# Optimization experiments

Measured on AMD Instinct MI355X. Metric: run time of the kernel, lower is better.

Reference implementation:

```python
import jax, jax.numpy as jnp
import numpy as np


def setup_inputs() -> dict:
    key = jax.random.key(0)
    ks = jax.random.split(key, 8)
    B, S, D, H, E = 4, 2048, 1024, 2048, 8
    s = 0.02  # init scale
    return {
        "x": jax.random.normal(ks[0], (B, S, D), dtype=jnp.float32),
        "gate_w": jax.random.normal(ks[1], (E, D), dtype=jnp.float32) * s,
        "w1": jax.random.normal(ks[2], (E, H, D), dtype=jnp.float32) * s,
        "b1": jnp.zeros((E, H), dtype=jnp.float32),
        "w2": jax.random.normal(ks[3], (E, H, D), dtype=jnp.float32) * s,
        "b2": jnp.zeros((E, H), dtype=jnp.float32),
        "w3": jax.random.normal(ks[4], (E, D, H), dtype=jnp.float32) * s,
        "b3": jnp.zeros((E, D), dtype=jnp.float32),
        "topk": 2,
    }


def reference(x, gate_w, w1, b1, w2, b2, w3, b3, topk):
    D = x.shape[-1]
    E = gate_w.shape[0]
    xf = x.reshape(-1, D)                      # [T, D]
    T = xf.shape[0]

    logits = xf @ gate_w.T                     # [T, E]
    vals, idx = jax.lax.top_k(logits, topk)    # [T, K]
    wts = jax.nn.softmax(vals, axis=-1)        # [T, K]

    # per-token combine weight per expert (0 if expert not in top-k)
    comb = jnp.zeros((T, E), dtype=xf.dtype).at[
        jnp.arange(T)[:, None], idx
    ].add(wts)                                 # [T, E]

    out = jnp.zeros_like(xf)
    for e in range(E):  # fixed small loop over experts
        h = (xf @ w1[e].T + b1[e]) * jax.nn.silu(xf @ w2[e].T + b2[e])  # [T, H]
        y = h @ w3[e].T + b3[e]                                           # [T, D]
        out = out + comb[:, e:e + 1] * y
    return out.reshape(x.shape)
```

## Files before the change

### kernel.cpp

```cpp
#include <hip/hip_runtime.h>
#include <hip/hip_bf16.h>
#include <stdint.h>

#define T_TOK   8192
#define D_DIM   1024
#define H_DIM   2048
#define E_EXP   8
#define NP2     4096
#define BM      256
#define CAP     (2*T_TOK + E_EXP*BM)
#define MAXMB   (CAP/BM)

using f32x4 = __attribute__((ext_vector_type(4))) float;
using s16x4 = __attribute__((ext_vector_type(4))) short;
using s16x8 = __attribute__((ext_vector_type(8))) short;

__device__ __forceinline__ short bf16_of(float f) {
  union { float f; unsigned u; } v; v.f = f;
  unsigned r = v.u + 0x7FFFu + ((v.u >> 16) & 1u);
  return (short)(r >> 16);
}
__device__ __forceinline__ float f_of_bf16(short s) {
  union { unsigned u; float f; } v; v.u = ((unsigned)(unsigned short)s) << 16;
  return v.f;
}

__device__ __forceinline__ void gload16(const void* g, void* l) {
  __builtin_amdgcn_global_load_lds(
      (const __attribute__((address_space(1))) unsigned int*)g,
      (__attribute__((address_space(3))) unsigned int*)l, 16, 0, 0);
}

__global__ __launch_bounds__(256) void conv_w12(const float* __restrict__ w1,
                                                const float* __restrict__ w2,
                                                short* __restrict__ w12b) {
  int idx = blockIdx.x * 256 + threadIdx.x;
  int e = idx >> 20;
  int rem = idx & 0xFFFFF;
  int np = rem >> 8;
  int kc = rem & 255;
  int g = np >> 5, tt = np & 31, half = tt >> 4, srow = g * 16 + (tt & 15);
  const f32x4* src = (const f32x4*)(half ? w2 : w1) + ((size_t)e * H_DIM + srow) * 256 + kc;
  f32x4 v = *src;
  s16x4 o;
  o[0] = bf16_of(v[0]); o[1] = bf16_of(v[1]); o[2] = bf16_of(v[2]); o[3] = bf16_of(v[3]);
  ((s16x4*)w12b)[idx] = o;
}

__global__ __launch_bounds__(256) void conv_w3(const float* __restrict__ w3,
                                               short* __restrict__ w3b) {
  int idx = blockIdx.x * 256 + threadIdx.x;
  f32x4 v = ((const f32x4*)w3)[idx];
  s16x4 o;
  o[0] = bf16_of(v[0]); o[1] = bf16_of(v[1]); o[2] = bf16_of(v[2]); o[3] = bf16_of(v[3]);
  ((s16x4*)w3b)[idx] = o;
}

__global__ __launch_bounds__(256) void gate_kernel(const float* __restrict__ x,
                                                   const float* __restrict__ gw,
                                                   int* __restrict__ tok_e,
                                                   float* __restrict__ gatew) {
  __shared__ float g[E_EXP * D_DIM];
  int tid = threadIdx.x;
  for (int i = tid; i < E_EXP * 256; i += 256)
    ((f32x4*)g)[i] = ((const f32x4*)gw)[i];
  __syncthreads();
  int w = tid >> 6, lane = tid & 63;
  int t = blockIdx.x * 4 + w;
  float acc[E_EXP] = {};
  const f32x4* xrow = (const f32x4*)(x + (size_t)t * D_DIM);
#pragma unroll
  for (int i = 0; i < 4; ++i) {
    f32x4 xv = xrow[lane + 64 * i];
#pragma unroll
    for (int e = 0; e < E_EXP; ++e) {
      f32x4 gv = ((const f32x4*)g)[e * 256 + lane + 64 * i];
      acc[e] += xv[0] * gv[0] + xv[1] * gv[1] + xv[2] * gv[2] + xv[3] * gv[3];
    }
  }
#pragma unroll
  for (int e = 0; e < E_EXP; ++e)
#pragma unroll
    for (int off = 1; off < 64; off <<= 1)
      acc[e] += __shfl_xor(acc[e], off);
  if (lane == 0) {
    int i0 = 0; float v0 = acc[0];
    for (int e = 1; e < E_EXP; ++e) if (acc[e] > v0) { v0 = acc[e]; i0 = e; }
    int i1 = -1; float v1 = -1e30f;
    for (int e = 0; e < E_EXP; ++e) if (e != i0 && acc[e] > v1) { v1 = acc[e]; i1 = e; }
    float z = __expf(v1 - v0);
    tok_e[2 * t] = i0; tok_e[2 * t + 1] = i1;
    gatew[2 * t] = 1.f / (1.f + z); gatew[2 * t + 1] = z / (1.f + z);
  }
}

__global__ __launch_bounds__(256) void hist_kernel(const int* __restrict__ tok_e,
                                                   int* __restrict__ counts) {
  __shared__ int bc[E_EXP];
  const int tid = threadIdx.x, lane = tid & 63;
  if (tid < E_EXP) bc[tid] = 0;
  __syncthreads();
  const int4 v = ((const int4*)tok_e)[blockIdx.x * 256 + tid];
#pragma unroll
  for (int e = 0; e < E_EXP; ++e) {
    int cnt = __popcll(__ballot(v.x == e)) + __popcll(__ballot(v.y == e)) +
              __popcll(__ballot(v.z == e)) + __popcll(__ballot(v.w == e));
    if (lane == 0 && cnt) atomicAdd(&bc[e], cnt);
  }
  __syncthreads();
  if (tid < E_EXP && bc[tid]) atomicAdd(&counts[tid], bc[tid]);
}

__global__ void scan_kernel(const int* __restrict__ counts, int* __restrict__ off,
                            int* __restrict__ mb2e, int* __restrict__ mb2row) {
  if (threadIdx.x == 0 && blockIdx.x == 0) {
    int acc = 0, mb = 0;
    for (int e = 0; e < E_EXP; ++e) {
      off[e] = acc;
      int nb = (counts[e] + BM - 1) / BM;
      for (int b = 0; b < nb; ++b) { mb2e[mb] = e; mb2row[mb] = acc + b * BM; ++mb; }
      acc += nb * BM;
    }
    off[E_EXP] = acc;
    for (; mb < MAXMB; ++mb) mb2e[mb] = -1;
  }
}

__global__ __launch_bounds__(256) void assign_kernel(const int* __restrict__ tok_e,
                                                     const int* __restrict__ off,
                                                     int* __restrict__ fill,
                                                     int* __restrict__ perm,
                                                     int* __restrict__ tok_slot) {
  __shared__ int wcnt[4][E_EXP];
  __shared__ int wbase[4][E_EXP];
  const int tid = threadIdx.x, lane = tid & 63, wid = tid >> 6;
  if (tid < 32) wcnt[tid >> 3][tid & 7] = 0;
  __syncthreads();
  const int ent = blockIdx.x * 256 + tid;
  const int e = tok_e[ent];
  int myrank = 0;
#pragma unroll
  for (int e0 = 0; e0 < E_EXP; ++e0) {
    unsigned long long m = __ballot(e == e0);
    if (e == e0) {
      myrank = __popcll(m & ((1ull << lane) - 1ull));
      if (myrank == 0) wcnt[wid][e0] = __popcll(m);
    }
  }
  __syncthreads();
  if (tid < E_EXP) {
    int tot = wcnt[0][tid] + wcnt[1][tid] + wcnt[2][tid] + wcnt[3][tid];
    int base = tot ? atomicAdd(&fill[tid], tot) : 0;
#pragma unroll
    for (int w = 0; w < 4; ++w) { wbase[w][tid] = base; base += wcnt[w][tid]; }
  }
  __syncthreads();
  const int slot = off[e] + wbase[wid][e] + myrank;
  perm[slot] = ent >> 1;
  tok_slot[ent] = slot;
}

__global__ __launch_bounds__(128) void gather_kernel(const float* __restrict__ x,
                                                     const int* __restrict__ off,
                                                     const int* __restrict__ counts,
                                                     const int* __restrict__ perm,
                                                     short* __restrict__ Xp) {
  int s = blockIdx.x, tid = threadIdx.x;
  int e = -1;
#pragma unroll
  for (int i = 0; i < E_EXP; ++i)
    if (s >= off[i] && s < off[i + 1]) { e = i; break; }
  bool valid = false; int t = 0;
  if (e >= 0) { int r = s - off[e]; if (r < counts[e]) { valid = true; t = perm[s]; } }
  s16x8 o;
  if (valid) {
    const f32x4* xr = (const f32x4*)(x + (size_t)t * D_DIM);
    f32x4 a = xr[tid * 2], b = xr[tid * 2 + 1];
    o[0] = bf16_of(a[0]); o[1] = bf16_of(a[1]); o[2] = bf16_of(a[2]); o[3] = bf16_of(a[3]);
    o[4] = bf16_of(b[0]); o[5] = bf16_of(b[1]); o[6] = bf16_of(b[2]); o[7] = bf16_of(b[3]);
  } else {
#pragma unroll
    for (int j = 0; j < 8; ++j) o[j] = 0;
  }
  *(s16x8*)(Xp + (size_t)s * D_DIM + tid * 8) = o;
}

template <int K, int EPI>
__global__ __launch_bounds__(512) void gemm256(const short* __restrict__ A,
                                               const short* __restrict__ Bw,
                                               const int* __restrict__ mb2e,
                                               const int* __restrict__ mb2row,
                                               const float* __restrict__ biasA,
                                               const float* __restrict__ biasB,
                                               short* __restrict__ Out) {
  constexpr int NFULL = (EPI == 0) ? NP2 : D_DIM;
  constexpr int OUTLD = (EPI == 0) ? H_DIM : D_DIM;
  constexpr int KB = K * 2;
  constexpr int NT = K / 32;

  const int mb = blockIdx.y;
  const int e = mb2e[mb];
  if (e < 0) return;
  const int row0 = mb2row[mb];
  const int bn = blockIdx.x;

  __shared__ alignas(16) char lds[3 * 32768];

  const int tid = threadIdx.x;
  const int lane = tid & 63;
  const int wid = tid >> 6;
  const int wr = wid >> 2;
  const int wc = wid & 3;

  const char* gA = (const char*)(A + (size_t)row0 * K);
  const char* gB = (const char*)(Bw + ((size_t)e * NFULL + (size_t)bn * BM) * K);

  const int srow0 = tid >> 2, spq = tid & 3;

  f32x4 acc[8][4] = {};

  auto stage = [&](int kt, int buf, int which) {
    const char* g = which ? gB : gA;
    char* l = lds + buf * 32768 + which * 16384;
#pragma unroll
    for (int rnd = 0; rnd < 2; ++rnd) {
      const int row = rnd * 128 + srow0;
      const int lq = spq ^ ((row >> 1) & 3);
      gload16(g + (size_t)row * KB + kt * 64 + lq * 16,
              l + rnd * 8192 + tid * 16);
    }
  };

  stage(0, 0, 0); stage(0, 0, 1);
  stage(1, 1, 0); stage(1, 1, 1);
  asm volatile("s_waitcnt vmcnt(4)" ::: "memory");
  __builtin_amdgcn_s_barrier();
  __builtin_amdgcn_sched_barrier(0);

  const int qsw = (((lane >> 4) ^ ((lane >> 1) & 3)) << 4);
  const int arow = wr * 128 + (lane & 15);
  const int brow = wc * 64 + (lane & 15);

  int bc = 0;
  int b2 = 2;
  for (int t = 0; t < NT; ++t) {
    const char* bufb = lds + bc * 32768;
    const char* pa = bufb + arow * 64 + qsw;
    const char* pb = bufb + 16384 + brow * 64 + qsw;
    s16x8 av[4], bv[4];
#pragma unroll
    for (int f = 0; f < 4; ++f) bv[f] = *(const s16x8*)(pb + f * 1024);
#pragma unroll
    for (int f = 0; f < 4; ++f) av[f] = *(const s16x8*)(pa + f * 1024);
    if (t + 2 < NT) stage(t + 2, b2, 0);
    __builtin_amdgcn_s_setprio(1);
#pragma unroll
    for (int mf = 0; mf < 4; ++mf)
#pragma unroll
      for (int nf = 0; nf < 4; ++nf)
        acc[mf][nf] = __builtin_amdgcn_mfma_f32_16x16x32_bf16(av[mf], bv[nf], acc[mf][nf], 0, 0, 0);
    __builtin_amdgcn_s_setprio(0);
#pragma unroll
    for (int f = 0; f < 4; ++f) av[f] = *(const s16x8*)(pa + (4 + f) * 1024);
    if (t + 2 < NT) stage(t + 2, b2, 1);
    __builtin_amdgcn_s_setprio(1);
#pragma unroll
    for (int mf = 0; mf < 4; ++mf)
#pragma unroll
      for (int nf = 0; nf < 4; ++nf)
        acc[4 + mf][nf] = __builtin_amdgcn_mfma_f32_16x16x32_bf16(av[mf], bv[nf], acc[4 + mf][nf], 0, 0, 0);
    __builtin_amdgcn_s_setprio(0);

    if (t < NT - 1) {
      __builtin_amdgcn_sched_barrier(0);
      if (t == NT - 2) asm volatile("s_waitcnt vmcnt(0)" ::: "memory");
      else             asm volatile("s_waitcnt vmcnt(4)" ::: "memory");
      __builtin_amdgcn_s_barrier();
      __builtin_amdgcn_sched_barrier(0);
    }
    bc = (bc == 2) ? 0 : bc + 1;
    b2 = (b2 == 2) ? 0 : b2 + 1;
  }

  if constexpr (EPI == 0) {
#pragma unroll
    for (int mf = 0; mf < 8; ++mf) {
      const int mrow = row0 + wr * 128 + mf * 16 + ((lane >> 4) << 2);
#pragma unroll
      for (int p = 0; p < 2; ++p) {
        const int hcol = bn * 128 + wc * 32 + p * 16 + (lane & 15);
        const float bb1 = biasA[e * H_DIM + hcol];
        const float bb2 = biasB[e * H_DIM + hcol];
        const f32x4 a1 = acc[mf][2 * p], a2 = acc[mf][2 * p + 1];
#pragma unroll
        for (int j = 0; j < 4; ++j) {
          float x1 = a1[j] + bb1, x2 = a2[j] + bb2;
          float hv = x1 * (x2 / (1.f + __expf(-x2)));
          Out[(size_t)(mrow + j) * OUTLD + hcol] = bf16_of(hv);
        }
      }
    }
  } else {
#pragma unroll
    for (int mf = 0; mf < 8; ++mf) {
      const int mrow = row0 + wr * 128 + mf * 16 + ((lane >> 4) << 2);
#pragma unroll
      for (int nf = 0; nf < 4; ++nf) {
        const int col = bn * BM + wc * 64 + nf * 16 + (lane & 15);
        const float bb = biasA[e * D_DIM + col];
#pragma unroll
        for (int j = 0; j < 4; ++j)
          Out[(size_t)(mrow + j) * OUTLD + col] = bf16_of(acc[mf][nf][j] + bb);
      }
    }
  }
}

__global__ __launch_bounds__(128) void combine_kernel(const short* __restrict__ ysb,
                                                      const int* __restrict__ tok_slot,
                                                      const float* __restrict__ gatew,
                                                      float* __restrict__ out) {
  int t = blockIdx.x, tid = threadIdx.x;
  int s0 = tok_slot[2 * t], s1 = tok_slot[2 * t + 1];
  float w0 = gatew[2 * t], w1 = gatew[2 * t + 1];
  s16x8 a = *(const s16x8*)(ysb + (size_t)s0 * D_DIM + tid * 8);
  s16x8 b = *(const s16x8*)(ysb + (size_t)s1 * D_DIM + tid * 8);
  float* op = out + (size_t)t * D_DIM + tid * 8;
  f32x4 o0, o1;
#pragma unroll
  for (int j = 0; j < 4; ++j) o0[j] = w0 * f_of_bf16(a[j]) + w1 * f_of_bf16(b[j]);
#pragma unroll
  for (int j = 0; j < 4; ++j) o1[j] = w0 * f_of_bf16(a[4 + j]) + w1 * f_of_bf16(b[4 + j]);
  *(f32x4*)op = o0;
  *(f32x4*)(op + 4) = o1;
}

extern "C" void kernel_launch(void* const* d_in, const int* in_sizes, int n_in,
                              void* d_out, int out_size, void* d_ws, size_t ws_size,
                              hipStream_t stream) {
  const float* x  = (const float*)d_in[0];
  const float* gw = (const float*)d_in[1];
  const float* w1 = (const float*)d_in[2];
  const float* b1 = (const float*)d_in[3];
  const float* w2 = (const float*)d_in[4];
  const float* b2 = (const float*)d_in[5];
  const float* w3 = (const float*)d_in[6];
  const float* b3 = (const float*)d_in[7];
  float* out = (float*)d_out;

  char* ws = (char*)d_ws;
  size_t o = 0;
  short* w12b = (short*)(ws + o); o += (size_t)E_EXP * NP2 * D_DIM * 2;
  short* w3b  = (short*)(ws + o); o += (size_t)E_EXP * D_DIM * H_DIM * 2;
  short* Xp   = (short*)(ws + o); o += (size_t)CAP * D_DIM * 2;
  short* ysb  = Xp;
  short* hbuf = (short*)(ws + o); o += (size_t)CAP * H_DIM * 2;
  int* meta     = (int*)(ws + o);
  int* counts   = meta;
  int* fill     = meta + 8;
  int* offv     = meta + 16;
  int* mb2e     = meta + 32;
  int* mb2row   = meta + 112;
  int* tok_e    = meta + 192;
  int* tok_slot = tok_e + 2 * T_TOK;
  int* perm     = tok_slot + 2 * T_TOK;
  float* gatew  = (float*)(perm + CAP);
  const size_t ws_needed = o + (192 + 4 * T_TOK + CAP + 2 * T_TOK) * sizeof(int);
  if (ws_size < ws_needed) return;

  hipMemsetAsync(counts, 0, 16 * sizeof(int), stream);

  conv_w12<<<(E_EXP * NP2 * 256) / 256, 256, 0, stream>>>(w1, w2, w12b);
  conv_w3 <<<(E_EXP * D_DIM * (H_DIM / 4)) / 256, 256, 0, stream>>>(w3, w3b);
  gate_kernel<<<T_TOK / 4, 256, 0, stream>>>(x, gw, tok_e, gatew);
  hist_kernel<<<(2 * T_TOK) / 1024, 256, 0, stream>>>(tok_e, counts);
  scan_kernel<<<1, 64, 0, stream>>>(counts, offv, mb2e, mb2row);
  assign_kernel<<<(2 * T_TOK) / 256, 256, 0, stream>>>(tok_e, offv, fill, perm, tok_slot);
  gather_kernel<<<CAP, 128, 0, stream>>>(x, offv, counts, perm, Xp);
  gemm256<D_DIM, 0><<<dim3(NP2 / BM, MAXMB), 512, 0, stream>>>(Xp, w12b, mb2e, mb2row, b1, b2, hbuf);
  gemm256<H_DIM, 1><<<dim3(D_DIM / BM, MAXMB), 512, 0, stream>>>(hbuf, w3b, mb2e, mb2row, b3, b3, ysb);
  combine_kernel<<<T_TOK, 128, 0, stream>>>(ysb, tok_slot, gatew, out);
}
```

Measured before the change: 376.0 us.

## Template GEMM on N tile width and add intra-iteration barriers for wave sync

Parameterizes the grouped GEMM on its N tile width and launches the down-projection with 128-wide tiles. This doubles the block count for the second GEMM and raises the occupancy hint, to fill more CUs on the smaller N=1024 output. It also adds s_barrier and lgkmcnt waits around each MFMA half-step so waves stay in lockstep, which may cost some overlap. With narrower tiles, each block reuses the A tile less, so A is read more times.

```diff
diff --git a/kernel.cpp b/kernel.cpp
--- a/kernel.cpp
+++ b/kernel.cpp
@@ -185,18 +185,24 @@
   *(s16x8*)(Xp + (size_t)s * D_DIM + tid * 8) = o;
 }
 
-template <int K, int EPI>
-__global__ __launch_bounds__(512) void gemm256(const short* __restrict__ A,
-                                               const short* __restrict__ Bw,
-                                               const int* __restrict__ mb2e,
-                                               const int* __restrict__ mb2row,
-                                               const float* __restrict__ biasA,
-                                               const float* __restrict__ biasB,
-                                               short* __restrict__ Out) {
+template <int K, int BN_, int EPI>
+__global__ __launch_bounds__(512, (BN_ == 128) ? 4 : 2)
+void gemm256(const short* __restrict__ A,
+             const short* __restrict__ Bw,
+             const int* __restrict__ mb2e,
+             const int* __restrict__ mb2row,
+             const float* __restrict__ biasA,
+             const float* __restrict__ biasB,
+             short* __restrict__ Out) {
   constexpr int NFULL = (EPI == 0) ? NP2 : D_DIM;
   constexpr int OUTLD = (EPI == 0) ? H_DIM : D_DIM;
   constexpr int KB = K * 2;
   constexpr int NT = K / 32;
+  constexpr int NBF = BN_ / 64;
+  constexpr int ABYTES = 16384;
+  constexpr int BBYTES = BN_ * 64;
+  constexpr int BUFB = ABYTES + BBYTES;
+  constexpr int NB_LOADS = BN_ / 128;
 
   const int mb = blockIdx.y;
   const int e = mb2e[mb];
@@ -204,7 +210,7 @@
   const int row0 = mb2row[mb];
   const int bn = blockIdx.x;
 
-  __shared__ alignas(16) char lds[3 * 32768];
+  __shared__ alignas(16) char lds[3 * BUFB];
 
   const int tid = threadIdx.x;
   const int lane = tid & 63;
@@ -213,68 +219,84 @@
   const int wc = wid & 3;
 
   const char* gA = (const char*)(A + (size_t)row0 * K);
-  const char* gB = (const char*)(Bw + ((size_t)e * NFULL + (size_t)bn * BM) * K);
+  const char* gB = (const char*)(Bw + ((size_t)e * NFULL + (size_t)bn * BN_) * K);
 
   const int srow0 = tid >> 2, spq = tid & 3;
 
-  f32x4 acc[8][4] = {};
-
-  auto stage = [&](int kt, int buf, int which) {
-    const char* g = which ? gB : gA;
-    char* l = lds + buf * 32768 + which * 16384;
-#pragma unroll
-    for (int rnd = 0; rnd < 2; ++rnd) {
-      const int row = rnd * 128 + srow0;
+  f32x4 acc[8][NBF] = {};
+
+  auto stageA = [&](int kt, int buf) {
+#pragma unroll
+    for (int r = 0; r < 2; ++r) {
+      const int row = r * 128 + srow0;
       const int lq = spq ^ ((row >> 1) & 3);
-      gload16(g + (size_t)row * KB + kt * 64 + lq * 16,
-              l + rnd * 8192 + tid * 16);
+      gload16(gA + (size_t)row * KB + kt * 64 + lq * 16,
+              lds + buf * BUFB + r * 8192 + tid * 16);
     }
   };
-
-  stage(0, 0, 0); stage(0, 0, 1);
-  stage(1, 1, 0); stage(1, 1, 1);
-  asm volatile("s_waitcnt vmcnt(4)" ::: "memory");
+  auto stageB = [&](int kt, int buf) {
+#pragma unroll
+    for (int r = 0; r < NB_LOADS; ++r) {
+      const int row = r * 128 + srow0;
+      const int lq = spq ^ ((row >> 1) & 3);
+      gload16(gB + (size_t)row * KB + kt * 64 + lq * 16,
+              lds + buf * BUFB + ABYTES + r * 8192 + tid * 16);
+    }
+  };
+
+  stageA(0, 0); stageB(0, 0);
+  stageA(1, 1); stageB(1, 1);
+  if constexpr (BN_ == 256) asm volatile("s_waitcnt vmcnt(4)" ::: "memory");
+  else                      asm volatile("s_waitcnt vmcnt(3)" ::: "memory");
   __builtin_amdgcn_s_barrier();
   __builtin_amdgcn_sched_barrier(0);
 
   const int qsw = (((lane >> 4) ^ ((lane >> 1) & 3)) << 4);
   const int arow = wr * 128 + (lane & 15);
-  const int brow = wc * 64 + (lane & 15);
+  const int brow = wc * (BN_ / 4) + (lane & 15);
 
   int bc = 0;
   int b2 = 2;
   for (int t = 0; t < NT; ++t) {
-    const char* bufb = lds + bc * 32768;
+    const char* bufb = lds + bc * BUFB;
     const char* pa = bufb + arow * 64 + qsw;
-    const char* pb = bufb + 16384 + brow * 64 + qsw;
-    s16x8 av[4], bv[4];
-#pragma unroll
-    for (int f = 0; f < 4; ++f) bv[f] = *(const s16x8*)(pb + f * 1024);
+    const char* pb = bufb + ABYTES + brow * 64 + qsw;
+    s16x8 av[4], bv[NBF];
+#pragma unroll
+    for (int f = 0; f < NBF; ++f) bv[f] = *(const s16x8*)(pb + f * 1024);
 #pragma unroll
     for (int f = 0; f < 4; ++f) av[f] = *(const s16x8*)(pa + f * 1024);
-    if (t + 2 < NT) stage(t + 2, b2, 0);
+    if (t + 2 < NT) stageA(t + 2, b2);
+    __builtin_amdgcn_s_barrier();
+    asm volatile("s_waitcnt lgkmcnt(0)" ::: "memory");
+    __builtin_amdgcn_sched_barrier(0);
     __builtin_amdgcn_s_setprio(1);
 #pragma unroll
     for (int mf = 0; mf < 4; ++mf)
 #pragma unroll
-      for (int nf = 0; nf < 4; ++nf)
+      for (int nf = 0; nf < NBF; ++nf)
         acc[mf][nf] = __builtin_amdgcn_mfma_f32_16x16x32_bf16(av[mf], bv[nf], acc[mf][nf], 0, 0, 0);
     __builtin_amdgcn_s_setprio(0);
+    __builtin_amdgcn_sched_barrier(0);
+    __builtin_amdgcn_s_barrier();
 #pragma unroll
     for (int f = 0; f < 4; ++f) av[f] = *(const s16x8*)(pa + (4 + f) * 1024);
-    if (t + 2 < NT) stage(t + 2, b2, 1);
+    if (t + 2 < NT) stageB(t + 2, b2);
+    __builtin_amdgcn_s_barrier();
+    asm volatile("s_waitcnt lgkmcnt(0)" ::: "memory");
+    __builtin_amdgcn_sched_barrier(0);
     __builtin_amdgcn_s_setprio(1);
 #pragma unroll
     for (int mf = 0; mf < 4; ++mf)
 #pragma unroll
-      for (int nf = 0; nf < 4; ++nf)
+      for (int nf = 0; nf < NBF; ++nf)
         acc[4 + mf][nf] = __builtin_amdgcn_mfma_f32_16x16x32_bf16(av[mf], bv[nf], acc[4 + mf][nf], 0, 0, 0);
     __builtin_amdgcn_s_setprio(0);
-
+    __builtin_amdgcn_sched_barrier(0);
     if (t < NT - 1) {
-      __builtin_amdgcn_sched_barrier(0);
-      if (t == NT - 2) asm volatile("s_waitcnt vmcnt(0)" ::: "memory");
-      else             asm volatile("s_waitcnt vmcnt(4)" ::: "memory");
+      if (t == NT - 2)          asm volatile("s_waitcnt vmcnt(0)" ::: "memory");
+      else if (BN_ == 256)      asm volatile("s_waitcnt vmcnt(4)" ::: "memory");
+      else                      asm volatile("s_waitcnt vmcnt(3)" ::: "memory");
       __builtin_amdgcn_s_barrier();
       __builtin_amdgcn_sched_barrier(0);
     }
@@ -305,8 +327,8 @@
     for (int mf = 0; mf < 8; ++mf) {
       const int mrow = row0 + wr * 128 + mf * 16 + ((lane >> 4) << 2);
 #pragma unroll
-      for (int nf = 0; nf < 4; ++nf) {
-        const int col = bn * BM + wc * 64 + nf * 16 + (lane & 15);
+      for (int nf = 0; nf < NBF; ++nf) {
+        const int col = bn * BN_ + wc * (BN_ / 4) + nf * 16 + (lane & 15);
         const float bb = biasA[e * D_DIM + col];
 #pragma unroll
         for (int j = 0; j < 4; ++j)
@@ -377,7 +399,7 @@
   scan_kernel<<<1, 64, 0, stream>>>(counts, offv, mb2e, mb2row);
   assign_kernel<<<(2 * T_TOK) / 256, 256, 0, stream>>>(tok_e, offv, fill, perm, tok_slot);
   gather_kernel<<<CAP, 128, 0, stream>>>(x, offv, counts, perm, Xp);
-  gemm256<D_DIM, 0><<<dim3(NP2 / BM, MAXMB), 512, 0, stream>>>(Xp, w12b, mb2e, mb2row, b1, b2, hbuf);
-  gemm256<H_DIM, 1><<<dim3(D_DIM / BM, MAXMB), 512, 0, stream>>>(hbuf, w3b, mb2e, mb2row, b3, b3, ysb);
+  gemm256<D_DIM, 256, 0><<<dim3(NP2 / 256, MAXMB), 512, 0, stream>>>(Xp, w12b, mb2e, mb2row, b1, b2, hbuf);
+  gemm256<H_DIM, 128, 1><<<dim3(D_DIM / 128, MAXMB), 512, 0, stream>>>(hbuf, w3b, mb2e, mb2row, b3, b3, ysb);
   combine_kernel<<<T_TOK, 128, 0, stream>>>(ysb, tok_slot, gatew, out);
 }
```

Measured after the change: 408.5 us. +8.7%, slower.

## Fuse fp32-to-bf16 weight conversion into grouped GEMM B-tile loading

Applied to the files above, without the earlier changes.

Drops the separate weight conversion kernels and bf16 weight buffers. The GEMMs now load fp32 weights straight into registers, convert them to bf16 and write them into swizzled LDS. The pipeline changes from a triple-buffered 32-wide K step with async global-to-LDS loads for both operands to a double-buffered 64-wide K step; only A still uses async LDS loads, and B is prefetched through registers. This saves a full pass over the weights, but every M-block now re-reads and re-converts fp32 weights, doubling weight bytes per tile, and the register-staged B path adds vmcnt stalls before each barrier.

```diff
diff --git a/kernel.cpp b/kernel.cpp
--- a/kernel.cpp
+++ b/kernel.cpp
@@ -12,7 +12,6 @@
 #define MAXMB   (CAP/BM)
 
 using f32x4 = __attribute__((ext_vector_type(4))) float;
-using s16x4 = __attribute__((ext_vector_type(4))) short;
 using s16x8 = __attribute__((ext_vector_type(8))) short;
 
 __device__ __forceinline__ short bf16_of(float f) {
@@ -29,31 +28,6 @@
   __builtin_amdgcn_global_load_lds(
       (const __attribute__((address_space(1))) unsigned int*)g,
       (__attribute__((address_space(3))) unsigned int*)l, 16, 0, 0);
-}
-
-__global__ __launch_bounds__(256) void conv_w12(const float* __restrict__ w1,
-                                                const float* __restrict__ w2,
-                                                short* __restrict__ w12b) {
-  int idx = blockIdx.x * 256 + threadIdx.x;
-  int e = idx >> 20;
-  int rem = idx & 0xFFFFF;
-  int np = rem >> 8;
-  int kc = rem & 255;
-  int g = np >> 5, tt = np & 31, half = tt >> 4, srow = g * 16 + (tt & 15);
-  const f32x4* src = (const f32x4*)(half ? w2 : w1) + ((size_t)e * H_DIM + srow) * 256 + kc;
-  f32x4 v = *src;
-  s16x4 o;
-  o[0] = bf16_of(v[0]); o[1] = bf16_of(v[1]); o[2] = bf16_of(v[2]); o[3] = bf16_of(v[3]);
-  ((s16x4*)w12b)[idx] = o;
-}
-
-__global__ __launch_bounds__(256) void conv_w3(const float* __restrict__ w3,
-                                               short* __restrict__ w3b) {
-  int idx = blockIdx.x * 256 + threadIdx.x;
-  f32x4 v = ((const f32x4*)w3)[idx];
-  s16x4 o;
-  o[0] = bf16_of(v[0]); o[1] = bf16_of(v[1]); o[2] = bf16_of(v[2]); o[3] = bf16_of(v[3]);
-  ((s16x4*)w3b)[idx] = o;
 }
 
 __global__ __launch_bounds__(256) void gate_kernel(const float* __restrict__ x,
@@ -186,17 +160,20 @@
 }
 
 template <int K, int EPI>
-__global__ __launch_bounds__(512) void gemm256(const short* __restrict__ A,
-                                               const short* __restrict__ Bw,
-                                               const int* __restrict__ mb2e,
-                                               const int* __restrict__ mb2row,
-                                               const float* __restrict__ biasA,
-                                               const float* __restrict__ biasB,
-                                               short* __restrict__ Out) {
-  constexpr int NFULL = (EPI == 0) ? NP2 : D_DIM;
-  constexpr int OUTLD = (EPI == 0) ? H_DIM : D_DIM;
+__global__ __launch_bounds__(512, 2)
+void gemm_fb(const short* __restrict__ A,
+             const float* __restrict__ Bw1,
+             const float* __restrict__ Bw2,
+             const int* __restrict__ mb2e,
+             const int* __restrict__ mb2row,
+             const float* __restrict__ biasA,
+             const float* __restrict__ biasB,
+             short* __restrict__ Out) {
   constexpr int KB = K * 2;
-  constexpr int NT = K / 32;
+  constexpr int NT = K / 64;
+  constexpr int HBYTES = 32768;
+  constexpr int BUFB = 2 * HBYTES;
+  constexpr int BSRCLD = (EPI == 0) ? D_DIM : H_DIM;
 
   const int mb = blockIdx.y;
   const int e = mb2e[mb];
@@ -204,7 +181,7 @@
   const int row0 = mb2row[mb];
   const int bn = blockIdx.x;
 
-  __shared__ alignas(16) char lds[3 * 32768];
+  __shared__ alignas(16) char lds[2 * BUFB];
 
   const int tid = threadIdx.x;
   const int lane = tid & 63;
@@ -213,73 +190,103 @@
   const int wc = wid & 3;
 
   const char* gA = (const char*)(A + (size_t)row0 * K);
-  const char* gB = (const char*)(Bw + ((size_t)e * NFULL + (size_t)bn * BM) * K);
-
-  const int srow0 = tid >> 2, spq = tid & 3;
+
+  const int browS = tid >> 1, bh = tid & 1;
+  const float* bsrc;
+  if constexpr (EPI == 0) {
+    const int np = bn * 256 + browS;
+    const int half = (np >> 4) & 1;
+    const int srow = (np >> 5) * 16 + (np & 15);
+    bsrc = (half ? Bw2 : Bw1) + ((size_t)e * H_DIM + srow) * BSRCLD;
+  } else {
+    bsrc = Bw1 + ((size_t)e * D_DIM + bn * 256 + browS) * BSRCLD;
+  }
+
+  f32x4 br[8];
+
+  auto loadB = [&](int kt) {
+    const f32x4* p = (const f32x4*)(bsrc + kt * 64 + bh * 32);
+#pragma unroll
+    for (int j = 0; j < 8; ++j) br[j] = p[j];
+  };
+  auto writeB = [&](int buf) {
+    char* l = lds + buf * BUFB + HBYTES + (size_t)browS * 128;
+#pragma unroll
+    for (int w = 0; w < 4; ++w) {
+      const f32x4 a = br[2 * w], b = br[2 * w + 1];
+      s16x8 o;
+      o[0] = bf16_of(a[0]); o[1] = bf16_of(a[1]); o[2] = bf16_of(a[2]); o[3] = bf16_of(a[3]);
+      o[4] = bf16_of(b[0]); o[5] = bf16_of(b[1]); o[6] = bf16_of(b[2]); o[7] = bf16_of(b[3]);
+      const int s = bh * 4 + w;
+      *(s16x8*)(l + ((s ^ (browS & 7)) * 16)) = o;
+    }
+  };
+  auto stageA = [&](int kt, int buf) {
+#pragma unroll
+    for (int r = 0; r < 4; ++r) {
+      const int row = r * 64 + (tid >> 3);
+      const int lq = (tid & 7) ^ (row & 7);
+      gload16(gA + (size_t)row * KB + kt * 128 + lq * 16,
+              lds + buf * BUFB + r * 8192 + tid * 16);
+    }
+  };
 
   f32x4 acc[8][4] = {};
 
-  auto stage = [&](int kt, int buf, int which) {
-    const char* g = which ? gB : gA;
-    char* l = lds + buf * 32768 + which * 16384;
-#pragma unroll
-    for (int rnd = 0; rnd < 2; ++rnd) {
-      const int row = rnd * 128 + srow0;
-      const int lq = spq ^ ((row >> 1) & 3);
-      gload16(g + (size_t)row * KB + kt * 64 + lq * 16,
-              l + rnd * 8192 + tid * 16);
-    }
-  };
-
-  stage(0, 0, 0); stage(0, 0, 1);
-  stage(1, 1, 0); stage(1, 1, 1);
-  asm volatile("s_waitcnt vmcnt(4)" ::: "memory");
+  loadB(0);
+  stageA(0, 0);
+  asm volatile("s_waitcnt vmcnt(0)" ::: "memory");
+  writeB(0);
+  asm volatile("s_waitcnt lgkmcnt(0)" ::: "memory");
   __builtin_amdgcn_s_barrier();
   __builtin_amdgcn_sched_barrier(0);
 
-  const int qsw = (((lane >> 4) ^ ((lane >> 1) & 3)) << 4);
   const int arow = wr * 128 + (lane & 15);
   const int brow = wc * 64 + (lane & 15);
-
-  int bc = 0;
-  int b2 = 2;
+  const int lsw = lane & 7;
+
   for (int t = 0; t < NT; ++t) {
-    const char* bufb = lds + bc * 32768;
-    const char* pa = bufb + arow * 64 + qsw;
-    const char* pb = bufb + 16384 + brow * 64 + qsw;
-    s16x8 av[4], bv[4];
-#pragma unroll
-    for (int f = 0; f < 4; ++f) bv[f] = *(const s16x8*)(pb + f * 1024);
-#pragma unroll
-    for (int f = 0; f < 4; ++f) av[f] = *(const s16x8*)(pa + f * 1024);
-    if (t + 2 < NT) stage(t + 2, b2, 0);
-    __builtin_amdgcn_s_setprio(1);
-#pragma unroll
-    for (int mf = 0; mf < 4; ++mf)
-#pragma unroll
-      for (int nf = 0; nf < 4; ++nf)
-        acc[mf][nf] = __builtin_amdgcn_mfma_f32_16x16x32_bf16(av[mf], bv[nf], acc[mf][nf], 0, 0, 0);
-    __builtin_amdgcn_s_setprio(0);
-#pragma unroll
-    for (int f = 0; f < 4; ++f) av[f] = *(const s16x8*)(pa + (4 + f) * 1024);
-    if (t + 2 < NT) stage(t + 2, b2, 1);
-    __builtin_amdgcn_s_setprio(1);
-#pragma unroll
-    for (int mf = 0; mf < 4; ++mf)
-#pragma unroll
-      for (int nf = 0; nf < 4; ++nf)
-        acc[4 + mf][nf] = __builtin_amdgcn_mfma_f32_16x16x32_bf16(av[mf], bv[nf], acc[4 + mf][nf], 0, 0, 0);
-    __builtin_amdgcn_s_setprio(0);
-
-    if (t < NT - 1) {
+    const char* bufb = lds + (t & 1) * BUFB;
+    const int nb = (t + 1) & 1;
+    const bool more = (t + 1 < NT);
+    if (more) loadB(t + 1);
+#pragma unroll
+    for (int ks = 0; ks < 2; ++ks) {
+      const int q = ((ks * 4 + (lane >> 4)) ^ lsw) * 16;
+      s16x8 av[4], bv[4];
+#pragma unroll
+      for (int f = 0; f < 4; ++f)
+        bv[f] = *(const s16x8*)(bufb + HBYTES + (size_t)(brow + f * 16) * 128 + q);
+#pragma unroll
+      for (int f = 0; f < 4; ++f)
+        av[f] = *(const s16x8*)(bufb + (size_t)(arow + f * 16) * 128 + q);
+      if (more && ks == 0) stageA(t + 1, nb);
+      __builtin_amdgcn_s_setprio(1);
+#pragma unroll
+      for (int mf = 0; mf < 4; ++mf)
+#pragma unroll
+        for (int nf = 0; nf < 4; ++nf)
+          acc[mf][nf] = __builtin_amdgcn_mfma_f32_16x16x32_bf16(av[mf], bv[nf], acc[mf][nf], 0, 0, 0);
+      __builtin_amdgcn_s_setprio(0);
+#pragma unroll
+      for (int f = 0; f < 4; ++f)
+        av[f] = *(const s16x8*)(bufb + (size_t)(arow + 64 + f * 16) * 128 + q);
+      __builtin_amdgcn_s_setprio(1);
+#pragma unroll
+      for (int mf = 0; mf < 4; ++mf)
+#pragma unroll
+        for (int nf = 0; nf < 4; ++nf)
+          acc[4 + mf][nf] = __builtin_amdgcn_mfma_f32_16x16x32_bf16(av[mf], bv[nf], acc[4 + mf][nf], 0, 0, 0);
+      __builtin_amdgcn_s_setprio(0);
+    }
+    if (more) {
       __builtin_amdgcn_sched_barrier(0);
-      if (t == NT - 2) asm volatile("s_waitcnt vmcnt(0)" ::: "memory");
-      else             asm volatile("s_waitcnt vmcnt(4)" ::: "memory");
+      asm volatile("s_waitcnt vmcnt(0)" ::: "memory");
+      writeB(nb);
+      asm volatile("s_waitcnt lgkmcnt(0)" ::: "memory");
       __builtin_amdgcn_s_barrier();
       __builtin_amdgcn_sched_barrier(0);
     }
-    bc = (bc == 2) ? 0 : bc + 1;
-    b2 = (b2 == 2) ? 0 : b2 + 1;
   }
 
   if constexpr (EPI == 0) {
@@ -296,7 +303,7 @@
         for (int j = 0; j < 4; ++j) {
           float x1 = a1[j] + bb1, x2 = a2[j] + bb2;
           float hv = x1 * (x2 / (1.f + __expf(-x2)));
-          Out[(size_t)(mrow + j) * OUTLD + hcol] = bf16_of(hv);
+          Out[(size_t)(mrow + j) * H_DIM + hcol] = bf16_of(hv);
         }
       }
     }
@@ -306,11 +313,11 @@
       const int mrow = row0 + wr * 128 + mf * 16 + ((lane >> 4) << 2);
 #pragma unroll
       for (int nf = 0; nf < 4; ++nf) {
-        const int col = bn * BM + wc * 64 + nf * 16 + (lane & 15);
+        const int col = bn * 256 + wc * 64 + nf * 16 + (lane & 15);
         const float bb = biasA[e * D_DIM + col];
 #pragma unroll
         for (int j = 0; j < 4; ++j)
-          Out[(size_t)(mrow + j) * OUTLD + col] = bf16_of(acc[mf][nf][j] + bb);
+          Out[(size_t)(mrow + j) * D_DIM + col] = bf16_of(acc[mf][nf][j] + bb);
       }
     }
   }
@@ -350,8 +357,6 @@
 
   char* ws = (char*)d_ws;
   size_t o = 0;
-  short* w12b = (short*)(ws + o); o += (size_t)E_EXP * NP2 * D_DIM * 2;
-  short* w3b  = (short*)(ws + o); o += (size_t)E_EXP * D_DIM * H_DIM * 2;
   short* Xp   = (short*)(ws + o); o += (size_t)CAP * D_DIM * 2;
   short* ysb  = Xp;
   short* hbuf = (short*)(ws + o); o += (size_t)CAP * H_DIM * 2;
@@ -370,14 +375,14 @@
 
   hipMemsetAsync(counts, 0, 16 * sizeof(int), stream);
 
-  conv_w12<<<(E_EXP * NP2 * 256) / 256, 256, 0, stream>>>(w1, w2, w12b);
-  conv_w3 <<<(E_EXP * D_DIM * (H_DIM / 4)) / 256, 256, 0, stream>>>(w3, w3b);
   gate_kernel<<<T_TOK / 4, 256, 0, stream>>>(x, gw, tok_e, gatew);
   hist_kernel<<<(2 * T_TOK) / 1024, 256, 0, stream>>>(tok_e, counts);
   scan_kernel<<<1, 64, 0, stream>>>(counts, offv, mb2e, mb2row);
   assign_kernel<<<(2 * T_TOK) / 256, 256, 0, stream>>>(tok_e, offv, fill, perm, tok_slot);
   gather_kernel<<<CAP, 128, 0, stream>>>(x, offv, counts, perm, Xp);
-  gemm256<D_DIM, 0><<<dim3(NP2 / BM, MAXMB), 512, 0, stream>>>(Xp, w12b, mb2e, mb2row, b1, b2, hbuf);
-  gemm256<H_DIM, 1><<<dim3(D_DIM / BM, MAXMB), 512, 0, stream>>>(hbuf, w3b, mb2e, mb2row, b3, b3, ysb);
+  gemm_fb<D_DIM, 0><<<dim3(NP2 / 256, MAXMB), 512, 0, stream>>>(
+      Xp, w1, w2, mb2e, mb2row, b1, b2, hbuf);
+  gemm_fb<H_DIM, 1><<<dim3(D_DIM / 256, MAXMB), 512, 0, stream>>>(
+      hbuf, w3, nullptr, mb2e, mb2row, b3, b3, ysb);
   combine_kernel<<<T_TOK, 128, 0, stream>>>(ysb, tok_slot, gatew, out);
 }
```

Result: slower. 565.5 us (+50.4%).
